# Optimization experiments

Measured on AMD Instinct MI355X. Metric: run time of the kernel, lower is better.

Reference implementation:

```python
import jax, jax.numpy as jnp
import numpy as np

B, C, Hh, Ww = 16, 256, 32, 32
HEADS = 4

def setup_inputs() -> dict:
    key = jax.random.key(0)
    ks = jax.random.split(key, 12)
    s = 0.02
    return {
        "x": jax.random.normal(ks[0], (B, C, Hh, Ww), jnp.float32),
        "q_w": jax.random.normal(ks[1], (C, C), jnp.float32) * s,
        "kv_w": jax.random.normal(ks[2], (2 * C, C), jnp.float32) * s,
        "proj_w": jax.random.normal(ks[3], (C, C), jnp.float32) * s,
        "proj_b": jnp.zeros((C,), jnp.float32),
        "lq_w": jax.random.normal(ks[4], (C, C), jnp.float32) * s,
        "lq_b": jnp.zeros((C,), jnp.float32),
        "lkv_w": jax.random.normal(ks[5], (2 * C, C), jnp.float32) * s,
        "lkv_b": jnp.zeros((2 * C,), jnp.float32),
        "rel_bias": jax.random.uniform(ks[6], (1, HEADS, 1, 1), jnp.float32),
        "dw_w": jax.random.normal(ks[7], (C, 1, 3, 3), jnp.float32) * s,
        "dw_b": jnp.zeros((C,), jnp.float32),
    }

def _forward(x, q_w, kv_w, proj_w, proj_b, lq_w, lq_b, lkv_w, lkv_b, rel_bias, dw_w, dw_b):
    b, c, h, w = x.shape
    N = h * w
    H = HEADS
    hd = c // H
    xf = x.reshape(b, c, N).transpose(0, 2, 1)  # [b, N, c]

    # ---- SRA (sr_ratio=1, no bias on q/kv) ----
    q = (xf @ q_w.T).reshape(b, N, H, hd).transpose(0, 2, 1, 3)          # [b,H,N,hd]
    kv = (xf @ kv_w.T).reshape(b, N, 2, H, hd).transpose(2, 0, 3, 1, 4)  # [2,b,H,N,hd]
    k, v = kv[0], kv[1]
    attn = jax.nn.softmax(jnp.einsum("bhqd,bhkd->bhqk", q, k) * (hd ** -0.5), axis=-1)
    y = jnp.einsum("bhqk,bhkd->bhqd", attn, v).transpose(0, 2, 1, 3).reshape(b, N, c)
    y = y @ proj_w.T + proj_b  # [b, N, c]

    # ---- depthwise conv on SRA output ----
    osr = y.transpose(0, 2, 1).reshape(b, c, h, w)
    osr = jax.lax.conv_general_dilated(
        osr, dw_w, window_strides=(1, 1), padding=((1, 1), (1, 1)),
        dimension_numbers=("NCHW", "OIHW", "NCHW"), feature_group_count=c)
    osr = osr + dw_b[None, :, None, None]
    osr = osr.reshape(b, c, N).transpose(0, 2, 1)  # [b, N, c]

    # ---- stage-2 attention with relative bias (faithful quirky reshape) ----
    q2 = (xf @ lq_w.T + lq_b).reshape(b, -1, 2, H, hd).transpose(2, 0, 3, 1, 4)  # [2,b,H,N/2,hd]
    kv2 = ((osr + y) @ lkv_w.T + lkv_b).reshape(b, -1, 2, H, hd).transpose(2, 0, 3, 1, 4)  # [2,b,H,N,hd]
    k2, v2 = kv2[0], kv2[1]
    d = hd ** 0.5
    scores = jnp.einsum("tbhqd,bhkd->tbhqk", q2, k2) / d + rel_bias  # [2,b,H,N/2,N]
    attn2 = jax.nn.softmax(scores, axis=-1)
    out = jnp.einsum("tbhqk,bhkd->tbhqd", attn2, v2)  # [2,b,H,N/2,hd]
    out = out.swapaxes(1, 2).reshape(b, N, c)          # torch .transpose(1,2)
    return out.reshape(b, h, w, c).transpose(0, 3, 1, 2)  # [b,c,h,w]

def reference(x, q_w, kv_w, proj_w, proj_b, lq_w, lq_b, lkv_w, lkv_b, rel_bias, dw_w, dw_b):
    return _forward(x, q_w, kv_w, proj_w, proj_b, lq_w, lq_b, lkv_w, lkv_b, rel_bias, dw_w, dw_b)
```

## Files before the change

### kernel.cpp

```cpp
#include <hip/hip_runtime.h>
#include <hip/hip_bf16.h>

#define B_  16
#define C_  256
#define N_  1024
#define H_  4

typedef unsigned short u16;
typedef __attribute__((ext_vector_type(8))) short bf16x8;
typedef __attribute__((ext_vector_type(4))) float f32x4;

#if __has_builtin(__builtin_amdgcn_exp2f)
#define EXP2(x) __builtin_amdgcn_exp2f(x)
#else
#define EXP2(x) __builtin_exp2f(x)
#endif

__device__ __forceinline__ u16 f2bf(float f) {
    union { float f; unsigned u; } v; v.f = f;
    unsigned r = v.u + 0x7FFFu + ((v.u >> 16) & 1u);
    return (u16)(r >> 16);
}
__device__ __forceinline__ float bf2f(u16 h) {
    union { unsigned u; float f; } v; v.u = ((unsigned)h) << 16;
    return v.f;
}
__device__ __forceinline__ unsigned pack2bf(float a, float b) {
    __hip_bfloat162 h = __float22bfloat162_rn(make_float2(a, b));
    union { __hip_bfloat162 h2; unsigned u; } cv; cv.h2 = h;
    return cv.u;
}
__device__ __forceinline__ void gl_lds16(const u16* g, u16* l) {
    __builtin_amdgcn_global_load_lds(
        (const __attribute__((address_space(1))) void*)g,
        (__attribute__((address_space(3))) void*)l, 16, 0, 0);
}

__global__ __launch_bounds__(256) void k_prep(const float* __restrict__ a0,
                                              const float* __restrict__ a1,
                                              const float* __restrict__ a2,
                                              const float* __restrict__ a3,
                                              const float* __restrict__ a4,
                                              u16* __restrict__ dst,
                                              const float* __restrict__ dw_w,
                                              float* __restrict__ wT,
                                              const float* __restrict__ x,
                                              u16* __restrict__ xf) {
    int blk = blockIdx.x;
    int t = threadIdx.x;
    if (blk < 448) {
        int i = blk * 256 + t;
        const float* s; int off;
        if (i < 16384)      { s = a0; off = 0; }
        else if (i < 49152) { s = a1; off = 16384; }
        else if (i < 65536) { s = a2; off = 49152; }
        else if (i < 81920) { s = a3; off = 65536; }
        else                { s = a4; off = 81920; }
        float4 v = reinterpret_cast<const float4*>(s)[i - off];
        ushort4 o;
        o.x = f2bf(v.x); o.y = f2bf(v.y); o.z = f2bf(v.z); o.w = f2bf(v.w);
        reinterpret_cast<ushort4*>(dst)[i] = o;
    } else if (blk == 448) {
#pragma unroll
        for (int tap = 0; tap < 9; tap++)
            wT[tap * 256 + t] = dw_w[t * 9 + tap];
    } else {
        __shared__ u16 tile[32][33];
        int f = blk - 449;
        int bx = f & 31, by = (f >> 5) & 7, b = f >> 8;
        int n0 = bx * 32, c0 = by * 32;
        int tx = t & 31, ty = t >> 5;
#pragma unroll
        for (int i = 0; i < 4; i++)
            tile[ty + i * 8][tx] =
                f2bf(x[((size_t)(b * C_ + c0 + ty + i * 8)) * N_ + n0 + tx]);
        __syncthreads();
#pragma unroll
        for (int i = 0; i < 4; i++)
            xf[((size_t)(b * N_ + n0 + ty + i * 8)) * C_ + c0 + tx] = tile[tx][ty + i * 8];
    }
}

__global__ __launch_bounds__(256) void k_packKV(const u16* __restrict__ src, int stride,
                                                u16* __restrict__ Kpk,
                                                u16* __restrict__ Vpk) {
    int blk = blockIdx.x;
    int t = threadIdx.x;
    if (blk < 2048) {
        const u16* Ksrc = src;
        int tid = blk * 256 + t;
        int lane = tid & 63;
        int chunk = tid >> 6;
        int c = chunk & 7;
        int kb = (chunk >> 3) & 15;
        int bh = chunk >> 7;
        int h = bh & 3, b = bh >> 2;
        int nt = c >> 1, w2 = c & 1;
        int l16 = lane & 15, g = lane >> 4;
        int rn = kb * 64 + (nt >> 1) * 32 + (nt & 1) * 4 + (((l16 & 12) << 1) | (l16 & 3));
        const u16* sp = Ksrc + (size_t)(b * N_ + rn) * stride + h * 64 + w2 * 32 + g * 8;
        *reinterpret_cast<bf16x8*>(&Kpk[(size_t)chunk * 512 + lane * 8]) =
            *reinterpret_cast<const bf16x8*>(sp);
    } else {
        __shared__ u16 tile[32][33];
        int f = blk - 2048;
        int bx = f & 31, by = (f >> 5) & 7, b = f >> 8;
        int n0 = bx * 32, vc0 = by * 32;
        int h = vc0 >> 6, dl = vc0 & 63;
        int bh = b * 4 + h;
        int kb = n0 >> 6, kc = (n0 >> 5) & 1;
        int tx = t & 31, ty = t >> 5;
        const u16* Vsrc = src + 256;
#pragma unroll
        for (int i = 0; i < 4; i++)
            tile[ty + i * 8][tx] =
                Vsrc[(size_t)(b * N_ + n0 + ty + i * 8) * stride + vc0 + tx];
        __syncthreads();
        int g = (tx >> 3) & 3, j = tx & 7;
#pragma unroll
        for (int i = 0; i < 4; i++) {
            int cl = ty + i * 8;
            int d = dl + cl;
            int dt = d >> 4;
            int lane = (d & 15) + 16 * g;
            size_t addr = ((size_t)(bh * 16 + kb) * 8 + kc * 4 + dt) * 512 + lane * 8 + j;
            Vpk[addr] = tile[tx][cl];
        }
    }
}

__global__ __launch_bounds__(256) void k_gemm_bf16(const u16* __restrict__ A, int astr,
                                                   const u16* __restrict__ W,
                                                   const float* __restrict__ bias,
                                                   int bofs, u16* __restrict__ C,
                                                   int Nout, int ldc) {
    __shared__ u16 As[128 * 32];
    __shared__ u16 Bs[128 * 32];
    int m0 = blockIdx.y * 128, n0 = blockIdx.x * 128;
    int t = threadIdx.x;
    int wid = t >> 6, lane = t & 63;
    int l16 = lane & 15, g = lane >> 4;
    int wm = (wid >> 1) * 64, wn = (wid & 1) * 64;
    int srow0 = (lane >> 2);
    int scol = (lane & 3) * 8;
    f32x4 zz = {0.f, 0.f, 0.f, 0.f};
    f32x4 acc[4][4];
#pragma unroll
    for (int i = 0; i < 4; i++)
#pragma unroll
        for (int j = 0; j < 4; j++) acc[i][j] = zz;
    for (int k0 = 0; k0 < 256; k0 += 32) {
        __syncthreads();
#pragma unroll
        for (int i = 0; i < 2; i++) {
            int rr = (wid * 2 + i) * 16;
            gl_lds16(A + (size_t)(m0 + rr + srow0) * astr + k0 + scol, &As[rr * 32]);
            gl_lds16(W + (size_t)(n0 + rr + srow0) * 256 + k0 + scol, &Bs[rr * 32]);
        }
        __syncthreads();
        bf16x8 af[4], bfr[4];
#pragma unroll
        for (int mt = 0; mt < 4; mt++)
            af[mt] = *reinterpret_cast<const bf16x8*>(&As[(wm + mt * 16 + l16) * 32 + g * 8]);
#pragma unroll
        for (int nt = 0; nt < 4; nt++)
            bfr[nt] = *reinterpret_cast<const bf16x8*>(&Bs[(wn + nt * 16 + l16) * 32 + g * 8]);
#pragma unroll
        for (int mt = 0; mt < 4; mt++)
#pragma unroll
            for (int nt = 0; nt < 4; nt++)
                acc[mt][nt] = __builtin_amdgcn_mfma_f32_16x16x32_bf16(
                    af[mt], bfr[nt], acc[mt][nt], 0, 0, 0);
    }
    float bval[4];
#pragma unroll
    for (int nt = 0; nt < 4; nt++) {
        int n = n0 + wn + nt * 16 + l16;
        bval[nt] = (bias && n >= bofs) ? bias[n - bofs] : 0.0f;
    }
#pragma unroll
    for (int mt = 0; mt < 4; mt++)
#pragma unroll
        for (int r = 0; r < 4; r++) {
            int m = m0 + wm + mt * 16 + g * 4 + r;
#pragma unroll
            for (int nt = 0; nt < 4; nt++) {
                int n = n0 + wn + nt * 16 + l16;
                C[(size_t)m * ldc + n] = f2bf(acc[mt][nt][r] + bval[nt]);
            }
        }
}

__global__ __launch_bounds__(256) void k_dwconv_add(const u16* __restrict__ yp,
                                                    const float* __restrict__ wT,
                                                    const float* __restrict__ dw_b,
                                                    u16* __restrict__ out) {
    int b = blockIdx.y;
    int px = blockIdx.x * 8 + (threadIdx.x >> 5);
    int cc0 = (threadIdx.x & 31) * 8;
    int yy = px >> 5, xx = px & 31;
    const u16* ypb = yp + (size_t)b * N_ * C_;
    float acc[8];
    {
        float4 b0 = *reinterpret_cast<const float4*>(&dw_b[cc0]);
        float4 b1 = *reinterpret_cast<const float4*>(&dw_b[cc0 + 4]);
        acc[0] = b0.x; acc[1] = b0.y; acc[2] = b0.z; acc[3] = b0.w;
        acc[4] = b1.x; acc[5] = b1.y; acc[6] = b1.z; acc[7] = b1.w;
    }
#pragma unroll
    for (int dy = 0; dy < 3; dy++) {
        int y2 = yy + dy - 1;
        if (y2 < 0 || y2 >= 32) continue;
#pragma unroll
        for (int dx = 0; dx < 3; dx++) {
            int x2 = xx + dx - 1;
            if (x2 < 0 || x2 >= 32) continue;
            int tap = dy * 3 + dx;
            bf16x8 v = *reinterpret_cast<const bf16x8*>(
                &ypb[(size_t)(y2 * 32 + x2) * C_ + cc0]);
            float4 w0 = *reinterpret_cast<const float4*>(&wT[tap * 256 + cc0]);
            float4 w1 = *reinterpret_cast<const float4*>(&wT[tap * 256 + cc0 + 4]);
            acc[0] += bf2f((u16)v[0]) * w0.x;
            acc[1] += bf2f((u16)v[1]) * w0.y;
            acc[2] += bf2f((u16)v[2]) * w0.z;
            acc[3] += bf2f((u16)v[3]) * w0.w;
            acc[4] += bf2f((u16)v[4]) * w1.x;
            acc[5] += bf2f((u16)v[5]) * w1.y;
            acc[6] += bf2f((u16)v[6]) * w1.z;
            acc[7] += bf2f((u16)v[7]) * w1.w;
        }
    }
    bf16x8 ctr = *reinterpret_cast<const bf16x8*>(&ypb[(size_t)px * C_ + cc0]);
    bf16x8 o;
#pragma unroll
    for (int j = 0; j < 8; j++)
        o[j] = (short)f2bf(acc[j] + bf2f((u16)ctr[j]));
    *reinterpret_cast<bf16x8*>(&out[((size_t)b * N_ + px) * C_ + cc0]) = o;
}

template <int STAGE>
__global__ __launch_bounds__(256, 4) void k_attn_mfma(const u16* __restrict__ Q, int qstr,
                                                      const u16* __restrict__ Kpk,
                                                      const u16* __restrict__ Vpk,
                                                      void* __restrict__ outp, int ostr) {
    __shared__ float Cmb[2][64][33];
    __shared__ float Clsum[2][64][2];
    int cid = blockIdx.x;
    int xcd = cid & 7, slot = cid >> 3;
    int bh = xcd * 8 + (slot & 7);
    int qc = slot >> 3;
    int h = bh & 3, b = bh >> 2;
    int t = threadIdx.x;
    int wv = t >> 6, lane = t & 63;
    int qpair = wv >> 1, kvh = wv & 1;
    int l16 = lane & 15, g = lane >> 4, g8 = g * 8;

    const float SCL = 0.18033688011112042f;
    const u16* Qb =
        Q + ((size_t)(b * N_ + qc * 64 + qpair * 32 + l16)) * qstr + h * 64 + g8;
    bf16x8 qf[2][2];
#pragma unroll
    for (int qg = 0; qg < 2; qg++)
#pragma unroll
        for (int w2 = 0; w2 < 2; w2++) {
            qf[qg][w2] = *reinterpret_cast<const bf16x8*>(Qb + qg * 16 * qstr + w2 * 32);
#pragma unroll
            for (int j = 0; j < 8; j++)
                qf[qg][w2][j] = (short)f2bf(bf2f((u16)qf[qg][w2][j]) * SCL);
        }

    const u16* Kp = Kpk + (size_t)bh * 65536 + lane * 8;
    const u16* Vp = Vpk + (size_t)bh * 65536 + lane * 8;

    int kb0 = kvh * 8, kb1 = kb0 + 8;
    bf16x8 kf[4][2];
#pragma unroll
    for (int nt = 0; nt < 4; nt++)
#pragma unroll
        for (int w2 = 0; w2 < 2; w2++)
            kf[nt][w2] = *reinterpret_cast<const bf16x8*>(
                Kp + (size_t)(kb0 * 8 + nt * 2 + w2) * 512);

    f32x4 zz = {0.f, 0.f, 0.f, 0.f};
    f32x4 accO[4][2];
#pragma unroll
    for (int dt = 0; dt < 4; dt++)
#pragma unroll
        for (int qg = 0; qg < 2; qg++) accO[dt][qg] = zz;
    float lsum[2] = {0.f, 0.f};
    int pwv[2][8];

    for (int kb = kb0; kb < kb1; kb++) {
        bf16x8 vf[2][4];
#pragma unroll
        for (int kc = 0; kc < 2; kc++)
#pragma unroll
            for (int dt = 0; dt < 4; dt++)
                vf[kc][dt] = *reinterpret_cast<const bf16x8*>(
                    Vp + (size_t)(kb * 8 + kc * 4 + dt) * 512);
#pragma unroll
        for (int qg = 0; qg < 2; qg++) {
            f32x4 st[4];
#pragma unroll
            for (int nt = 0; nt < 4; nt++) st[nt] = zz;
#pragma unroll
            for (int nt = 0; nt < 4; nt++) {
                st[nt] = __builtin_amdgcn_mfma_f32_16x16x32_bf16(kf[nt][0], qf[qg][0],
                                                                 st[nt], 0, 0, 0);
                st[nt] = __builtin_amdgcn_mfma_f32_16x16x32_bf16(kf[nt][1], qf[qg][1],
                                                                 st[nt], 0, 0, 0);
            }
#pragma unroll
            for (int nt = 0; nt < 4; nt++) {
                float p0 = EXP2(st[nt][0]);
                float p1 = EXP2(st[nt][1]);
                float p2 = EXP2(st[nt][2]);
                float p3 = EXP2(st[nt][3]);
                lsum[qg] += (p0 + p1) + (p2 + p3);
                pwv[qg][nt * 2 + 0] = (int)pack2bf(p0, p1);
                pwv[qg][nt * 2 + 1] = (int)pack2bf(p2, p3);
            }
        }
        {
            int nkb = (kb < kb1 - 1) ? kb + 1 : kb;
#pragma unroll
            for (int nt = 0; nt < 4; nt++)
#pragma unroll
                for (int w2 = 0; w2 < 2; w2++)
                    kf[nt][w2] = *reinterpret_cast<const bf16x8*>(
                        Kp + (size_t)(nkb * 8 + nt * 2 + w2) * 512);
        }
#pragma unroll
        for (int qg = 0; qg < 2; qg++)
#pragma unroll
            for (int kc = 0; kc < 2; kc++) {
                union { int i[4]; bf16x8 v; } u;
                u.i[0] = pwv[qg][4 * kc + 0];
                u.i[1] = pwv[qg][4 * kc + 1];
                u.i[2] = pwv[qg][4 * kc + 2];
                u.i[3] = pwv[qg][4 * kc + 3];
#pragma unroll
                for (int dt = 0; dt < 4; dt++)
                    accO[dt][qg] = __builtin_amdgcn_mfma_f32_16x16x32_bf16(
                        vf[kc][dt], u.v, accO[dt][qg], 0, 0, 0);
            }
    }

    if (kvh == 1) {
#pragma unroll
        for (int dt = 0; dt < 4; dt++)
#pragma unroll
            for (int qg = 0; qg < 2; qg++)
#pragma unroll
                for (int r = 0; r < 4; r++)
                    Cmb[qpair][lane][(dt * 2 + qg) * 4 + r] = accO[dt][qg][r];
        Clsum[qpair][lane][0] = lsum[0];
        Clsum[qpair][lane][1] = lsum[1];
    }
    __syncthreads();
    if (kvh == 0) {
#pragma unroll
        for (int dt = 0; dt < 4; dt++)
#pragma unroll
            for (int qg = 0; qg < 2; qg++)
#pragma unroll
                for (int r = 0; r < 4; r++)
                    accO[dt][qg][r] += Cmb[qpair][lane][(dt * 2 + qg) * 4 + r];
        lsum[0] += Clsum[qpair][lane][0];
        lsum[1] += Clsum[qpair][lane][1];
        float inv[2];
#pragma unroll
        for (int qg = 0; qg < 2; qg++) {
            float l = lsum[qg];
            l += __shfl_xor(l, 16);
            l += __shfl_xor(l, 32);
            inv[qg] = 1.0f / l;
        }
        if constexpr (STAGE == 0) {
            u16* O = (u16*)outp;
            size_t rowb = (size_t)(b * N_ + qc * 64 + qpair * 32 + l16);
#pragma unroll
            for (int qg = 0; qg < 2; qg++)
#pragma unroll
                for (int dt = 0; dt < 4; dt++) {
                    ushort4 o;
                    o.x = f2bf(accO[dt][qg][0] * inv[qg]);
                    o.y = f2bf(accO[dt][qg][1] * inv[qg]);
                    o.z = f2bf(accO[dt][qg][2] * inv[qg]);
                    o.w = f2bf(accO[dt][qg][3] * inv[qg]);
                    *reinterpret_cast<ushort4*>(
                        &O[(rowb + qg * 16) * ostr + h * 64 + dt * 16 + g * 4]) = o;
                }
        }
    }
    if constexpr (STAGE == 1) {
        __shared__ float Os[64][68];
        if (kvh == 0) {
            float inv[2];
#pragma unroll
            for (int qg = 0; qg < 2; qg++) {
                float l = lsum[qg];
                l += __shfl_xor(l, 16);
                l += __shfl_xor(l, 32);
                inv[qg] = 1.0f / l;
            }
            int qrl = qpair * 32 + l16;
#pragma unroll
            for (int qg = 0; qg < 2; qg++)
#pragma unroll
                for (int dt = 0; dt < 4; dt++)
#pragma unroll
                    for (int r = 0; r < 4; r++)
                        Os[qrl + qg * 16][dt * 16 + g * 4 + r] = accO[dt][qg][r] * inv[qg];
        }
        __syncthreads();
        float* out = (float*)outp;
#pragma unroll
        for (int e = 0; e < 2; e++) {
            int seg = t + e * 256;
            int d = seg & 63, tb = seg >> 6;
            int tl = tb & 1, q2 = (tb >> 1) & 3;
            int bo = tl * 8 + h * 2 + (b >> 3);
            int co = q2 * 64 + d;
            size_t base = (size_t)bo * (C_ * N_) + (size_t)co * N_ + (b & 7) * 128 + qc * 8;
            float4 v0, v1;
            v0.x = Os[0 * 8 + q2 * 2 + tl][d];
            v0.y = Os[1 * 8 + q2 * 2 + tl][d];
            v0.z = Os[2 * 8 + q2 * 2 + tl][d];
            v0.w = Os[3 * 8 + q2 * 2 + tl][d];
            v1.x = Os[4 * 8 + q2 * 2 + tl][d];
            v1.y = Os[5 * 8 + q2 * 2 + tl][d];
            v1.z = Os[6 * 8 + q2 * 2 + tl][d];
            v1.w = Os[7 * 8 + q2 * 2 + tl][d];
            *reinterpret_cast<float4*>(&out[base]) = v0;
            *reinterpret_cast<float4*>(&out[base + 4]) = v1;
        }
    }
}

extern "C" void kernel_launch(void* const* d_in, const int* in_sizes, int n_in,
                              void* d_out, int out_size, void* d_ws, size_t ws_size,
                              hipStream_t stream) {
    const float* x      = (const float*)d_in[0];
    const float* q_w    = (const float*)d_in[1];
    const float* kv_w   = (const float*)d_in[2];
    const float* proj_w = (const float*)d_in[3];
    const float* proj_b = (const float*)d_in[4];
    const float* lq_w   = (const float*)d_in[5];
    const float* lq_b   = (const float*)d_in[6];
    const float* lkv_w  = (const float*)d_in[7];
    const float* lkv_b  = (const float*)d_in[8];
    const float* dw_w   = (const float*)d_in[10];
    const float* dw_b   = (const float*)d_in[11];

    const size_t SZ = (size_t)B_ * N_ * C_;
    u16* ws = (u16*)d_ws;
    u16* xf    = ws;
    u16* qkv   = ws + SZ;
    u16* Kpk   = ws + 5 * SZ;
    u16* Vpk   = ws + 6 * SZ;
    u16* arena = ws + 7 * SZ;
    u16* wmega  = arena;
    u16* wproj  = arena + 262144;
    u16* wlkv   = arena + 327680;
    float* wT   = (float*)(arena + 458752);
    u16* yb     = qkv + 256;
    u16* ypb    = Kpk;
    u16* s2in   = xf;

    k_prep<<<4545, 256, 0, stream>>>(q_w, kv_w, lq_w, proj_w, lkv_w, arena,
                                     dw_w, wT, x, xf);
    k_gemm_bf16<<<dim3(8, 128), 256, 0, stream>>>(xf, 256, wmega, lq_b, 768,
                                                  qkv, 1024, 1024);
    k_packKV<<<6144, 256, 0, stream>>>(qkv + 256, 1024, Kpk, Vpk);
    k_attn_mfma<0><<<1024, 256, 0, stream>>>(qkv, 1024, Kpk, Vpk, yb, 1024);
    k_gemm_bf16<<<dim3(2, 128), 256, 0, stream>>>(yb, 1024, wproj, proj_b, 0,
                                                  ypb, 256, 256);
    k_dwconv_add<<<dim3(128, B_), 256, 0, stream>>>(ypb, wT, dw_b, s2in);
    k_gemm_bf16<<<dim3(4, 128), 256, 0, stream>>>(s2in, 256, wlkv, lkv_b, 0,
                                                  qkv + 256, 512, 1024);
    k_packKV<<<6144, 256, 0, stream>>>(qkv + 256, 1024, Kpk, Vpk);
    k_attn_mfma<1><<<1024, 256, 0, stream>>>(qkv + 768, 1024, Kpk, Vpk, d_out, 0);
}
```

Baseline: 136.7 us.

## Fuse K/V packing into GEMM epilogue and drop packKV kernels

The GEMM epilogue now writes the K and V column ranges directly into the packed MFMA-friendly Kpk/Vpk layouts the attention kernel expects. This removes both k_packKV launches and their extra global read/write passes over the K/V activations. In exchange, epilogue stores become more scattered for those column blocks, and the GEMM gains branching and index arithmetic.

```diff
diff --git a/kernel.cpp b/kernel.cpp
--- a/kernel.cpp
+++ b/kernel.cpp
@@ -81,59 +81,13 @@
     }
 }
 
-__global__ __launch_bounds__(256) void k_packKV(const u16* __restrict__ src, int stride,
-                                                u16* __restrict__ Kpk,
-                                                u16* __restrict__ Vpk) {
-    int blk = blockIdx.x;
-    int t = threadIdx.x;
-    if (blk < 2048) {
-        const u16* Ksrc = src;
-        int tid = blk * 256 + t;
-        int lane = tid & 63;
-        int chunk = tid >> 6;
-        int c = chunk & 7;
-        int kb = (chunk >> 3) & 15;
-        int bh = chunk >> 7;
-        int h = bh & 3, b = bh >> 2;
-        int nt = c >> 1, w2 = c & 1;
-        int l16 = lane & 15, g = lane >> 4;
-        int rn = kb * 64 + (nt >> 1) * 32 + (nt & 1) * 4 + (((l16 & 12) << 1) | (l16 & 3));
-        const u16* sp = Ksrc + (size_t)(b * N_ + rn) * stride + h * 64 + w2 * 32 + g * 8;
-        *reinterpret_cast<bf16x8*>(&Kpk[(size_t)chunk * 512 + lane * 8]) =
-            *reinterpret_cast<const bf16x8*>(sp);
-    } else {
-        __shared__ u16 tile[32][33];
-        int f = blk - 2048;
-        int bx = f & 31, by = (f >> 5) & 7, b = f >> 8;
-        int n0 = bx * 32, vc0 = by * 32;
-        int h = vc0 >> 6, dl = vc0 & 63;
-        int bh = b * 4 + h;
-        int kb = n0 >> 6, kc = (n0 >> 5) & 1;
-        int tx = t & 31, ty = t >> 5;
-        const u16* Vsrc = src + 256;
-#pragma unroll
-        for (int i = 0; i < 4; i++)
-            tile[ty + i * 8][tx] =
-                Vsrc[(size_t)(b * N_ + n0 + ty + i * 8) * stride + vc0 + tx];
-        __syncthreads();
-        int g = (tx >> 3) & 3, j = tx & 7;
-#pragma unroll
-        for (int i = 0; i < 4; i++) {
-            int cl = ty + i * 8;
-            int d = dl + cl;
-            int dt = d >> 4;
-            int lane = (d & 15) + 16 * g;
-            size_t addr = ((size_t)(bh * 16 + kb) * 8 + kc * 4 + dt) * 512 + lane * 8 + j;
-            Vpk[addr] = tile[tx][cl];
-        }
-    }
-}
-
 __global__ __launch_bounds__(256) void k_gemm_bf16(const u16* __restrict__ A, int astr,
                                                    const u16* __restrict__ W,
                                                    const float* __restrict__ bias,
                                                    int bofs, u16* __restrict__ C,
-                                                   int Nout, int ldc) {
+                                                   int ldc,
+                                                   u16* __restrict__ Kpk, int kpk_lo,
+                                                   u16* __restrict__ Vpk, int vpk_lo) {
     __shared__ u16 As[128 * 32];
     __shared__ u16 Bs[128 * 32];
     int m0 = blockIdx.y * 128, n0 = blockIdx.x * 128;
@@ -178,17 +132,65 @@
         int n = n0 + wn + nt * 16 + l16;
         bval[nt] = (bias && n >= bofs) ? bias[n - bofs] : 0.0f;
     }
-#pragma unroll
-    for (int mt = 0; mt < 4; mt++)
-#pragma unroll
-        for (int r = 0; r < 4; r++) {
-            int m = m0 + wm + mt * 16 + g * 4 + r;
-#pragma unroll
-            for (int nt = 0; nt < 4; nt++) {
-                int n = n0 + wn + nt * 16 + l16;
-                C[(size_t)m * ldc + n] = f2bf(acc[mt][nt][r] + bval[nt]);
-            }
-        }
+    bool kpack = (n0 >= kpk_lo) && (n0 < kpk_lo + 256);
+    bool vpack = (n0 >= vpk_lo) && (n0 < vpk_lo + 256);
+    if (kpack) {
+        int hcol = n0 - kpk_lo + wn;
+#pragma unroll
+        for (int mt = 0; mt < 4; mt++)
+#pragma unroll
+            for (int r = 0; r < 4; r++) {
+                int m = m0 + wm + mt * 16 + g * 4 + r;
+                int b = m >> 10, rn = m & 1023;
+                int kb = rn >> 6, r6 = rn & 63;
+                int nt2 = ((r6 >> 5) << 1) | ((r6 >> 2) & 1);
+                int l2 = (r6 & 3) | ((r6 >> 1) & 12);
+#pragma unroll
+                for (int nt = 0; nt < 4; nt++) {
+                    int c = hcol + nt * 16 + l16;
+                    int h = c >> 6, c6 = c & 63;
+                    int w2 = c6 >> 5, g2 = (c6 >> 3) & 3, j = c6 & 7;
+                    size_t chunk = ((size_t)(b * 4 + h) * 16 + kb) * 8 + nt2 * 2 + w2;
+                    Kpk[chunk * 512 + (l2 + 16 * g2) * 8 + j] =
+                        f2bf(acc[mt][nt][r] + bval[nt]);
+                }
+            }
+    } else if (vpack) {
+        int hcol = n0 - vpk_lo + wn;
+#pragma unroll
+        for (int mt = 0; mt < 4; mt++)
+#pragma unroll
+            for (int r = 0; r < 4; r++) {
+                int m = m0 + wm + mt * 16 + g * 4 + r;
+                int b = m >> 10;
+                int kv = m & 1023;
+                int kb = kv >> 6;
+                int kc = (kv >> 5) & 1;
+                int g3 = (kv >> 3) & 3;
+                int j = kv & 7;
+#pragma unroll
+                for (int nt = 0; nt < 4; nt++) {
+                    int c = hcol + nt * 16 + l16;
+                    int h = c >> 6, d6 = c & 63;
+                    int dt = d6 >> 4, d15 = d6 & 15;
+                    size_t chunk = ((size_t)(b * 4 + h) * 16 + kb) * 8 + kc * 4 + dt;
+                    Vpk[chunk * 512 + (d15 + 16 * g3) * 8 + j] =
+                        f2bf(acc[mt][nt][r] + bval[nt]);
+                }
+            }
+    } else {
+#pragma unroll
+        for (int mt = 0; mt < 4; mt++)
+#pragma unroll
+            for (int r = 0; r < 4; r++) {
+                int m = m0 + wm + mt * 16 + g * 4 + r;
+#pragma unroll
+                for (int nt = 0; nt < 4; nt++) {
+                    int n = n0 + wn + nt * 16 + l16;
+                    C[(size_t)m * ldc + n] = f2bf(acc[mt][nt][r] + bval[nt]);
+                }
+            }
+    }
 }
 
 __global__ __launch_bounds__(256) void k_dwconv_add(const u16* __restrict__ yp,
@@ -467,18 +469,17 @@
     u16* yb     = qkv + 256;
     u16* ypb    = Kpk;
     u16* s2in   = xf;
+    const int DIS = 1 << 30;
 
     k_prep<<<4545, 256, 0, stream>>>(q_w, kv_w, lq_w, proj_w, lkv_w, arena,
                                      dw_w, wT, x, xf);
     k_gemm_bf16<<<dim3(8, 128), 256, 0, stream>>>(xf, 256, wmega, lq_b, 768,
-                                                  qkv, 1024, 1024);
-    k_packKV<<<6144, 256, 0, stream>>>(qkv + 256, 1024, Kpk, Vpk);
+                                                  qkv, 1024, Kpk, 256, Vpk, 512);
     k_attn_mfma<0><<<1024, 256, 0, stream>>>(qkv, 1024, Kpk, Vpk, yb, 1024);
     k_gemm_bf16<<<dim3(2, 128), 256, 0, stream>>>(yb, 1024, wproj, proj_b, 0,
-                                                  ypb, 256, 256);
+                                                  ypb, 256, nullptr, DIS, nullptr, DIS);
     k_dwconv_add<<<dim3(128, B_), 256, 0, stream>>>(ypb, wT, dw_b, s2in);
     k_gemm_bf16<<<dim3(4, 128), 256, 0, stream>>>(s2in, 256, wlkv, lkv_b, 0,
-                                                  qkv + 256, 512, 1024);
-    k_packKV<<<6144, 256, 0, stream>>>(qkv + 256, 1024, Kpk, Vpk);
+                                                  qkv, 1024, Kpk, 0, Vpk, 256);
     k_attn_mfma<1><<<1024, 256, 0, stream>>>(qkv + 768, 1024, Kpk, Vpk, d_out, 0);
 }
```

Result: faster. 130.1 us (median of 2 runs) (-4.8%).
